# Kernel tuning notes

Hardware: AMD Instinct MI355X
Metric: run time of the kernel (lower is better)

The kernel has to match this reference:

```python
import jax, jax.numpy as jnp
import numpy as np

HIDDEN = 32  # hard-coded in the module


def _lstm_cell(x, h, c, W_ih, W_hh, b_ih, b_hh):
    # torch.nn.LSTMCell: gates in order i, f, g, o
    gates = x @ W_ih.T + b_ih + h @ W_hh.T + b_hh
    i, f, g, o = jnp.split(gates, 4, axis=-1)
    c_new = jax.nn.sigmoid(f) * c + jax.nn.sigmoid(i) * jnp.tanh(g)
    h_new = jax.nn.sigmoid(o) * jnp.tanh(c_new)
    return h_new, c_new


def setup_inputs() -> dict:
    key = jax.random.key(0)
    ks = jax.random.split(key, 11)
    B, T, d, len_out = 256, 1024, 8, 10
    s = 0.05
    return {
        "input": jax.random.normal(ks[0], (B, T, d), dtype=jnp.float32),
        "W_ih1": jax.random.normal(ks[1], (4 * HIDDEN, d), dtype=jnp.float32) * s,
        "W_hh1": jax.random.normal(ks[2], (4 * HIDDEN, HIDDEN), dtype=jnp.float32) * s,
        "b_ih1": jax.random.normal(ks[3], (4 * HIDDEN,), dtype=jnp.float32) * s,
        "b_hh1": jax.random.normal(ks[4], (4 * HIDDEN,), dtype=jnp.float32) * s,
        "W_ih2": jax.random.normal(ks[5], (4 * HIDDEN, HIDDEN), dtype=jnp.float32) * s,
        "W_hh2": jax.random.normal(ks[6], (4 * HIDDEN, HIDDEN), dtype=jnp.float32) * s,
        "b_ih2": jax.random.normal(ks[7], (4 * HIDDEN,), dtype=jnp.float32) * s,
        "b_hh2": jax.random.normal(ks[8], (4 * HIDDEN,), dtype=jnp.float32) * s,
        "W_lin": jax.random.normal(ks[9], (d * len_out, HIDDEN), dtype=jnp.float32) * s,
        "b_lin": jax.random.normal(ks[10], (d * len_out,), dtype=jnp.float32) * s,
    }


def reference(input, W_ih1, W_hh1, b_ih1, b_hh1, W_ih2, W_hh2, b_ih2, b_hh2, W_lin, b_lin):
    B, T, d = input.shape
    len_out = W_lin.shape[0] // d

    def step(carry, x_t):
        h1, c1, h2, c2 = carry
        h1, c1 = _lstm_cell(x_t, h1, c1, W_ih1, W_hh1, b_ih1, b_hh1)
        h2, c2 = _lstm_cell(h1, h2, c2, W_ih2, W_hh2, b_ih2, b_hh2)
        out = h2 @ W_lin.T + b_lin  # [B, d*len_out]
        return (h1, c1, h2, c2), out

    z = jnp.zeros((B, HIDDEN), dtype=input.dtype)
    init = (z, z, z, z)
    xs = jnp.swapaxes(input, 0, 1)  # [T, B, d]
    _, outs = jax.lax.scan(step, init, xs)  # [T, B, d*len_out]
    outs = jnp.swapaxes(outs, 0, 1)  # [B, T, d*len_out]
    return outs.reshape(B, T, d, len_out)
```

## Files before the change

kernel.cpp:

```cpp
#include <hip/hip_runtime.h>

#define TT  1024
#define DIN 8

__device__ __forceinline__ float fsig(float x) {
    float e = __builtin_amdgcn_exp2f(-1.4426950408889634f * x);
    return __builtin_amdgcn_rcpf(1.0f + e);
}
__device__ __forceinline__ float ftanh_(float x) {
    float e = __builtin_amdgcn_exp2f(-2.8853900817779268f * x);
    return 2.0f * __builtin_amdgcn_rcpf(1.0f + e) - 1.0f;
}
template<int CTRL>
__device__ __forceinline__ float dppf(float v) {
    return __uint_as_float((unsigned)__builtin_amdgcn_update_dpp(
        0, (int)__float_as_uint(v), CTRL, 0xF, 0xF, true));
}
__device__ __forceinline__ void bar_lgkm() {
    asm volatile("s_waitcnt lgkmcnt(0)\n\ts_barrier" ::: "memory");
}

__global__ void __launch_bounds__(512, 2)
lstm_pipe8(const float* __restrict__ x,
           const float* __restrict__ Wih1, const float* __restrict__ Whh1,
           const float* __restrict__ bih1, const float* __restrict__ bhh1,
           const float* __restrict__ Wih2, const float* __restrict__ Whh2,
           const float* __restrict__ bih2, const float* __restrict__ bhh2,
           const float* __restrict__ Wlin, const float* __restrict__ blin,
           float* __restrict__ out)
{
    const int tid  = threadIdx.x;
    const int wv   = tid >> 6;
    const int l    = tid & 63;
    const int part = l & 1;
    const int g    = (l >> 1) & 3;
    const int ul   = l >> 3;
    const int b    = blockIdx.x;
    const bool isL1 = (wv < 4);
    const int  wu   = isL1 ? wv : (wv - 4);
    const int  unit = wu*8 + ul;
    const int  R    = g*32 + unit;
    const bool isg  = (g == 2);

    __shared__ float hb1[2][32];
    __shared__ float hb2[2][32];
    if (tid < 64)       ((float*)hb1)[tid]      = 0.f;
    else if (tid < 128) ((float*)hb2)[tid - 64] = 0.f;

    float wg[20];
    float wg2[32];
    float wl[16];
    float bias = 0.f, obias = 0.f;
    int ocol = 0;

    if (isL1) {
        const float* wsrc = Whh1 + R*32 + part*16;
#pragma unroll
        for (int qq = 0; qq < 4; ++qq) {
            float4 v = reinterpret_cast<const float4*>(wsrc)[qq];
            wg[4*qq]=v.x; wg[4*qq+1]=v.y; wg[4*qq+2]=v.z; wg[4*qq+3]=v.w;
        }
        float4 xv = *reinterpret_cast<const float4*>(Wih1 + R*DIN + part*4);
        wg[16]=xv.x; wg[17]=xv.y; wg[18]=xv.z; wg[19]=xv.w;
        if (!part) bias = bih1[R] + bhh1[R];
        ocol = wu*20 + (l >> 1);
        const int oc = (l < 40) ? ocol : 79;
        const float* osrc = Wlin + oc*32 + part*16;
#pragma unroll
        for (int qq = 0; qq < 4; ++qq) {
            float4 v = reinterpret_cast<const float4*>(osrc)[qq];
            wl[4*qq]=v.x; wl[4*qq+1]=v.y; wl[4*qq+2]=v.z; wl[4*qq+3]=v.w;
        }
        if (!part) obias = blin[oc];
    } else {
        const float* wsrc = part ? (Wih2 + R*32) : (Whh2 + R*32);
#pragma unroll
        for (int qq = 0; qq < 8; ++qq) {
            float4 v = reinterpret_cast<const float4*>(wsrc)[qq];
            wg2[4*qq]=v.x; wg2[4*qq+1]=v.y; wg2[4*qq+2]=v.z; wg2[4*qq+3]=v.w;
        }
        if (!part) bias = bih2[R] + bhh2[R];
    }

    float c = 0.f;

    const float* __restrict__ xb = x   + (size_t)b * (TT*DIN);
    float* __restrict__ outb     = out + (size_t)b * (TT*80);

    float4 xcur;
    if (isL1) xcur = *reinterpret_cast<const float4*>(xb + part*4);

    bar_lgkm();

#pragma unroll 1
    for (int t = 0; t <= TT + 1; ++t) {
        const int pm1 = (t - 1) & 1;
        const int p0  = t & 1;

        if (isL1) {
            const float* hin = &hb1[pm1][part << 4];
            const float* hob = &hb2[p0][part << 4];
            float4 hg[4], ho[4];
#pragma unroll
            for (int qq = 0; qq < 4; ++qq) hg[qq] = reinterpret_cast<const float4*>(hin)[qq];
#pragma unroll
            for (int qq = 0; qq < 4; ++qq) ho[qq] = reinterpret_cast<const float4*>(hob)[qq];

            if (t < TT) {
                float a0 = bias, a1 = 0.f, a2 = 0.f, a3 = 0.f;
#pragma unroll
                for (int qq = 0; qq < 4; ++qq) {
                    a0 += wg[4*qq]  *hg[qq].x; a1 += wg[4*qq+1]*hg[qq].y;
                    a2 += wg[4*qq+2]*hg[qq].z; a3 += wg[4*qq+3]*hg[qq].w;
                }
                a0 += wg[16]*xcur.x; a1 += wg[17]*xcur.y;
                a2 += wg[18]*xcur.z; a3 += wg[19]*xcur.w;
                const int tn = (t + 1 < TT) ? (t + 1) : (TT - 1);
                xcur = *reinterpret_cast<const float4*>(xb + tn*DIN + part*4);

                float sum  = (a0 + a1) + (a2 + a3);
                float full = sum + dppf<0xB1>(sum);
                float u  = isg ? (full + full) : full;
                float S  = fsig(u);
                float av = isg ? (S + S - 1.0f) : S;
                float itg = dppf<0x114>(av) * av;
                float fv  = dppf<0x112>(av);
                c = fv * c + itg;
                float so  = dppf<0x102>(av);
                float hv  = so * ftanh_(c);
                if ((l & 7) == 4) hb1[p0][unit] = hv;
            }
            if (t >= 2) {
                float o0 = obias, o1 = 0.f, o2 = 0.f, o3 = 0.f;
#pragma unroll
                for (int qq = 0; qq < 4; ++qq) {
                    o0 += wl[4*qq]  *ho[qq].x; o1 += wl[4*qq+1]*ho[qq].y;
                    o2 += wl[4*qq+2]*ho[qq].z; o3 += wl[4*qq+3]*ho[qq].w;
                }
                float osum  = (o0 + o1) + (o2 + o3);
                float ofull = osum + dppf<0xB1>(osum);
                if (!part && l < 40)
                    outb[(size_t)(t - 2)*80 + ocol] = ofull;
            }
        } else {
            if (t >= 1 && t <= TT) {
                const float* hin = part ? &hb1[pm1][0] : &hb2[p0][0];
                float a0 = bias, a1 = 0.f, a2 = 0.f, a3 = 0.f;
#pragma unroll
                for (int qq = 0; qq < 8; ++qq) {
                    float4 v = reinterpret_cast<const float4*>(hin)[qq];
                    a0 += wg2[4*qq]  *v.x; a1 += wg2[4*qq+1]*v.y;
                    a2 += wg2[4*qq+2]*v.z; a3 += wg2[4*qq+3]*v.w;
                }
                float sum  = (a0 + a1) + (a2 + a3);
                float full = sum + dppf<0xB1>(sum);
                float u  = isg ? (full + full) : full;
                float S  = fsig(u);
                float av = isg ? (S + S - 1.0f) : S;
                float itg = dppf<0x114>(av) * av;
                float fv  = dppf<0x112>(av);
                c = fv * c + itg;
                float so  = dppf<0x102>(av);
                float hv  = so * ftanh_(c);
                if ((l & 7) == 4) hb2[pm1][unit] = hv;
            }
        }

        bar_lgkm();
    }
}

extern "C" void kernel_launch(void* const* d_in, const int* in_sizes, int n_in,
                              void* d_out, int out_size, void* d_ws, size_t ws_size,
                              hipStream_t stream) {
    const float* x    = (const float*)d_in[0];
    const float* Wih1 = (const float*)d_in[1];
    const float* Whh1 = (const float*)d_in[2];
    const float* bih1 = (const float*)d_in[3];
    const float* bhh1 = (const float*)d_in[4];
    const float* Wih2 = (const float*)d_in[5];
    const float* Whh2 = (const float*)d_in[6];
    const float* bih2 = (const float*)d_in[7];
    const float* bhh2 = (const float*)d_in[8];
    const float* Wlin = (const float*)d_in[9];
    const float* blin = (const float*)d_in[10];

    const int B = in_sizes[0] / (TT * DIN);

    hipLaunchKernelGGL(lstm_pipe8, dim3(B), dim3(512), 0, stream,
                       x, Wih1, Whh1, bih1, bhh1,
                       Wih2, Whh2, bih2, bhh2, Wlin, blin,
                       (float*)d_out);
}
```

Before: 464.8 us.

## Restructure LSTM kernel into per-wave roles handling two batch elements per block

Each 512-thread block now processes two batch elements, with four waves per element split into roles: a single wave for layer 1, two waves for layer 2, and one wave for the output projection. Layer 1 keeps its hidden state in registers and broadcasts it with readlane, so its recurrence no longer round-trips through LDS. The time loop is unrolled by two with ping-pong buffers. The aim is to shorten the per-step critical path and halve the grid, at the cost of more registers and more readlane work per step.

```diff
diff --git a/kernel.cpp b/kernel.cpp
--- a/kernel.cpp
+++ b/kernel.cpp
@@ -10,6 +10,9 @@
 __device__ __forceinline__ float ftanh_(float x) {
     float e = __builtin_amdgcn_exp2f(-2.8853900817779268f * x);
     return 2.0f * __builtin_amdgcn_rcpf(1.0f + e) - 1.0f;
+}
+__device__ __forceinline__ float bcastf(float v, int k) {
+    return __uint_as_float((unsigned)__builtin_amdgcn_readlane((int)__float_as_uint(v), k));
 }
 template<int CTRL>
 __device__ __forceinline__ float dppf(float v) {
@@ -19,9 +22,100 @@
 __device__ __forceinline__ void bar_lgkm() {
     asm volatile("s_waitcnt lgkmcnt(0)\n\ts_barrier" ::: "memory");
 }
+__device__ __forceinline__ void row32g(const float* __restrict__ p, float* r) {
+#pragma unroll
+    for (int qq = 0; qq < 8; ++qq) {
+        float4 v = reinterpret_cast<const float4*>(p)[qq];
+        r[4*qq]=v.x; r[4*qq+1]=v.y; r[4*qq+2]=v.z; r[4*qq+3]=v.w;
+    }
+}
+__device__ __forceinline__ void lds32(const float* p, float* r) {
+#pragma unroll
+    for (int qq = 0; qq < 8; ++qq) {
+        float4 v = reinterpret_cast<const float4*>(p)[qq];
+        r[4*qq]=v.x; r[4*qq+1]=v.y; r[4*qq+2]=v.z; r[4*qq+3]=v.w;
+    }
+}
+
+#define L1STEP(X0, X1, PAR)                                                   \
+    {                                                                         \
+        float p0a = bq0, p0b = 0.f, p1a = bq1, p1b = 0.f;                     \
+        _Pragma("unroll")                                                     \
+        for (int k = 0; k < 32; k += 2) {                                     \
+            p0a += wh0[k]*hs[k];   p0b += wh0[k+1]*hs[k+1];                   \
+            p1a += wh1[k]*hs[k];   p1b += wh1[k+1]*hs[k+1];                   \
+        }                                                                     \
+        p0a += wx0[0]*X0.x; p0b += wx0[1]*X0.y;                               \
+        p0a += wx0[2]*X0.z; p0b += wx0[3]*X0.w;                               \
+        p0a += wx0[4]*X1.x; p0b += wx0[5]*X1.y;                               \
+        p0a += wx0[6]*X1.z; p0b += wx0[7]*X1.w;                               \
+        p1a += wx1[0]*X0.x; p1b += wx1[1]*X0.y;                               \
+        p1a += wx1[2]*X0.z; p1b += wx1[3]*X0.w;                               \
+        p1a += wx1[4]*X1.x; p1b += wx1[5]*X1.y;                               \
+        p1a += wx1[6]*X1.z; p1b += wx1[7]*X1.w;                               \
+        float pp0 = p0a + p0b, pp1 = p1a + p1b;                               \
+        float A  = fsig(pp0);                                                 \
+        float uu = q ? pp1 : (pp1 + pp1);                                     \
+        float S  = fsig(uu);                                                  \
+        float Bv = q ? S : (S + S - 1.0f);                                    \
+        float An = dppf<0xB1>(A), Bn = dppf<0xB1>(Bv);                        \
+        float si = q ? An : A,  sf = q ? A  : An;                             \
+        float tg = q ? Bn : Bv, so = q ? Bv : Bn;                             \
+        c1 = sf * c1 + si * tg;                                               \
+        float h1v = so * ftanh_(c1);                                          \
+        if (!q) hb1[elem][PAR][j] = h1v;                                      \
+        _Pragma("unroll")                                                     \
+        for (int k = 0; k < 32; ++k) hs[k] = bcastf(h1v, 2*k);                \
+    }
+
+#define L2STEP(PT)                                                            \
+    {                                                                         \
+        float h1l = hb1[elem][PT][l & 31];                                    \
+        float h2r_[32];                                                       \
+        lds32(&hb2[elem][(PT)^1][0], h2r_);                                   \
+        float h1s_[32];                                                       \
+        _Pragma("unroll")                                                     \
+        for (int k = 0; k < 32; ++k) h1s_[k] = bcastf(h1l, k);                \
+        float a0 = bq, a1 = 0.f, a2 = 0.f, a3 = 0.f;                          \
+        _Pragma("unroll")                                                     \
+        for (int k = 0; k < 32; k += 4) {                                     \
+            a0 += w2[k]  *h1s_[k];   a1 += w2[k+1]*h1s_[k+1];                 \
+            a2 += w2[k+2]*h1s_[k+2]; a3 += w2[k+3]*h1s_[k+3];                 \
+        }                                                                     \
+        _Pragma("unroll")                                                     \
+        for (int k = 0; k < 32; k += 4) {                                     \
+            a0 += u2[k]  *h2r_[k];   a1 += u2[k+1]*h2r_[k+1];                 \
+            a2 += u2[k+2]*h2r_[k+2]; a3 += u2[k+3]*h2r_[k+3];                 \
+        }                                                                     \
+        float gg = (a0 + a1) + (a2 + a3);                                     \
+        float uu = isg ? (gg + gg) : gg;                                      \
+        float S  = fsig(uu);                                                  \
+        float av = isg ? (S + S - 1.0f) : S;                                  \
+        float siq = dppf<0x00>(av);                                           \
+        float sfq = dppf<0x55>(av);                                           \
+        float tgq = dppf<0xAA>(av);                                           \
+        float soq = dppf<0xFF>(av);                                           \
+        c2 = sfq * c2 + siq * tgq;                                            \
+        float h2v = soq * ftanh_(c2);                                         \
+        if (g == 0) hb2[elem][PT][u] = h2v;                                   \
+    }
+
+#define OUTSTEP(TAU, PT)                                                      \
+    {                                                                         \
+        float h2r_[32];                                                       \
+        lds32(&hb2[elem][PT][0], h2r_);                                       \
+        float o0 = bo0, o1 = 0.f, po0 = bo1, po1 = 0.f;                       \
+        _Pragma("unroll")                                                     \
+        for (int k = 0; k < 32; k += 2) {                                     \
+            o0  += wl0[k]*h2r_[k];  o1  += wl0[k+1]*h2r_[k+1];                \
+            po0 += wl1[k]*h2r_[k];  po1 += wl1[k+1]*h2r_[k+1];                \
+        }                                                                     \
+        outb[(size_t)(TAU)*80 + c0] = o0 + o1;                                \
+        if (l < 16) outb[(size_t)(TAU)*80 + 64 + l] = po0 + po1;              \
+    }
 
 __global__ void __launch_bounds__(512, 2)
-lstm_pipe8(const float* __restrict__ x,
+lstm_roles(const float* __restrict__ x,
            const float* __restrict__ Wih1, const float* __restrict__ Whh1,
            const float* __restrict__ bih1, const float* __restrict__ bhh1,
            const float* __restrict__ Wih2, const float* __restrict__ Whh2,
@@ -32,140 +126,103 @@
     const int tid  = threadIdx.x;
     const int wv   = tid >> 6;
     const int l    = tid & 63;
-    const int part = l & 1;
-    const int g    = (l >> 1) & 3;
-    const int ul   = l >> 3;
-    const int b    = blockIdx.x;
-    const bool isL1 = (wv < 4);
-    const int  wu   = isL1 ? wv : (wv - 4);
-    const int  unit = wu*8 + ul;
-    const int  R    = g*32 + unit;
-    const bool isg  = (g == 2);
-
-    __shared__ float hb1[2][32];
-    __shared__ float hb2[2][32];
-    if (tid < 64)       ((float*)hb1)[tid]      = 0.f;
-    else if (tid < 128) ((float*)hb2)[tid - 64] = 0.f;
-
-    float wg[20];
-    float wg2[32];
-    float wl[16];
-    float bias = 0.f, obias = 0.f;
-    int ocol = 0;
-
-    if (isL1) {
-        const float* wsrc = Whh1 + R*32 + part*16;
-#pragma unroll
-        for (int qq = 0; qq < 4; ++qq) {
-            float4 v = reinterpret_cast<const float4*>(wsrc)[qq];
-            wg[4*qq]=v.x; wg[4*qq+1]=v.y; wg[4*qq+2]=v.z; wg[4*qq+3]=v.w;
-        }
-        float4 xv = *reinterpret_cast<const float4*>(Wih1 + R*DIN + part*4);
-        wg[16]=xv.x; wg[17]=xv.y; wg[18]=xv.z; wg[19]=xv.w;
-        if (!part) bias = bih1[R] + bhh1[R];
-        ocol = wu*20 + (l >> 1);
-        const int oc = (l < 40) ? ocol : 79;
-        const float* osrc = Wlin + oc*32 + part*16;
-#pragma unroll
-        for (int qq = 0; qq < 4; ++qq) {
-            float4 v = reinterpret_cast<const float4*>(osrc)[qq];
-            wl[4*qq]=v.x; wl[4*qq+1]=v.y; wl[4*qq+2]=v.z; wl[4*qq+3]=v.w;
-        }
-        if (!part) obias = blin[oc];
-    } else {
-        const float* wsrc = part ? (Wih2 + R*32) : (Whh2 + R*32);
-#pragma unroll
-        for (int qq = 0; qq < 8; ++qq) {
-            float4 v = reinterpret_cast<const float4*>(wsrc)[qq];
-            wg2[4*qq]=v.x; wg2[4*qq+1]=v.y; wg2[4*qq+2]=v.z; wg2[4*qq+3]=v.w;
-        }
-        if (!part) bias = bih2[R] + bhh2[R];
-    }
-
-    float c = 0.f;
+    const int role = wv & 3;
+    const int elem = wv >> 2;
+    const int b    = blockIdx.x * 2 + elem;
+
+    __shared__ __align__(16) float hb1[2][2][32];
+    __shared__ __align__(16) float hb2[2][2][32];
+    if (tid < 128)      ((float*)hb1)[tid]       = 0.f;
+    else if (tid < 256) ((float*)hb2)[tid - 128] = 0.f;
 
     const float* __restrict__ xb = x   + (size_t)b * (TT*DIN);
     float* __restrict__ outb     = out + (size_t)b * (TT*80);
 
-    float4 xcur;
-    if (isL1) xcur = *reinterpret_cast<const float4*>(xb + part*4);
-
-    bar_lgkm();
+    if (role == 0) {
+        const int q = l & 1, j = l >> 1;
+        const int r0 = q ? (32 + j) : j;
+        const int r1 = q ? (96 + j) : (64 + j);
+        float wx0[8], wx1[8];
+#pragma unroll
+        for (int k = 0; k < 8; ++k) { wx0[k] = Wih1[r0*8+k]; wx1[k] = Wih1[r1*8+k]; }
+        float wh0[32], wh1[32];
+        row32g(Whh1 + r0*32, wh0); row32g(Whh1 + r1*32, wh1);
+        const float bq0 = bih1[r0] + bhh1[r0];
+        const float bq1 = bih1[r1] + bhh1[r1];
+        float hs[32];
+#pragma unroll
+        for (int k = 0; k < 32; ++k) hs[k] = 0.f;
+        float c1 = 0.f;
+        float4 xA0 = reinterpret_cast<const float4*>(xb)[0];
+        float4 xA1 = reinterpret_cast<const float4*>(xb)[1];
+        float4 xB0 = reinterpret_cast<const float4*>(xb)[2];
+        float4 xB1 = reinterpret_cast<const float4*>(xb)[3];
+
+        bar_lgkm();
 
 #pragma unroll 1
-    for (int t = 0; t <= TT + 1; ++t) {
-        const int pm1 = (t - 1) & 1;
-        const int p0  = t & 1;
-
-        if (isL1) {
-            const float* hin = &hb1[pm1][part << 4];
-            const float* hob = &hb2[p0][part << 4];
-            float4 hg[4], ho[4];
-#pragma unroll
-            for (int qq = 0; qq < 4; ++qq) hg[qq] = reinterpret_cast<const float4*>(hin)[qq];
-#pragma unroll
-            for (int qq = 0; qq < 4; ++qq) ho[qq] = reinterpret_cast<const float4*>(hob)[qq];
-
-            if (t < TT) {
-                float a0 = bias, a1 = 0.f, a2 = 0.f, a3 = 0.f;
-#pragma unroll
-                for (int qq = 0; qq < 4; ++qq) {
-                    a0 += wg[4*qq]  *hg[qq].x; a1 += wg[4*qq+1]*hg[qq].y;
-                    a2 += wg[4*qq+2]*hg[qq].z; a3 += wg[4*qq+3]*hg[qq].w;
-                }
-                a0 += wg[16]*xcur.x; a1 += wg[17]*xcur.y;
-                a2 += wg[18]*xcur.z; a3 += wg[19]*xcur.w;
-                const int tn = (t + 1 < TT) ? (t + 1) : (TT - 1);
-                xcur = *reinterpret_cast<const float4*>(xb + tn*DIN + part*4);
-
-                float sum  = (a0 + a1) + (a2 + a3);
-                float full = sum + dppf<0xB1>(sum);
-                float u  = isg ? (full + full) : full;
-                float S  = fsig(u);
-                float av = isg ? (S + S - 1.0f) : S;
-                float itg = dppf<0x114>(av) * av;
-                float fv  = dppf<0x112>(av);
-                c = fv * c + itg;
-                float so  = dppf<0x102>(av);
-                float hv  = so * ftanh_(c);
-                if ((l & 7) == 4) hb1[p0][unit] = hv;
+        for (int tp = 0; tp < TT/2; ++tp) {
+            const int te = 2*tp;
+            L1STEP(xA0, xA1, 0)
+            {
+                const int tn = (te + 2 <= TT - 1) ? (te + 2) : 0;
+                xA0 = reinterpret_cast<const float4*>(xb + tn*DIN)[0];
+                xA1 = reinterpret_cast<const float4*>(xb + tn*DIN)[1];
             }
-            if (t >= 2) {
-                float o0 = obias, o1 = 0.f, o2 = 0.f, o3 = 0.f;
-#pragma unroll
-                for (int qq = 0; qq < 4; ++qq) {
-                    o0 += wl[4*qq]  *ho[qq].x; o1 += wl[4*qq+1]*ho[qq].y;
-                    o2 += wl[4*qq+2]*ho[qq].z; o3 += wl[4*qq+3]*ho[qq].w;
-                }
-                float osum  = (o0 + o1) + (o2 + o3);
-                float ofull = osum + dppf<0xB1>(osum);
-                if (!part && l < 40)
-                    outb[(size_t)(t - 2)*80 + ocol] = ofull;
+            bar_lgkm();
+            L1STEP(xB0, xB1, 1)
+            {
+                const int tn = (te + 3 <= TT - 1) ? (te + 3) : 0;
+                xB0 = reinterpret_cast<const float4*>(xb + tn*DIN)[0];
+                xB1 = reinterpret_cast<const float4*>(xb + tn*DIN)[1];
             }
-        } else {
-            if (t >= 1 && t <= TT) {
-                const float* hin = part ? &hb1[pm1][0] : &hb2[p0][0];
-                float a0 = bias, a1 = 0.f, a2 = 0.f, a3 = 0.f;
-#pragma unroll
-                for (int qq = 0; qq < 8; ++qq) {
-                    float4 v = reinterpret_cast<const float4*>(hin)[qq];
-                    a0 += wg2[4*qq]  *v.x; a1 += wg2[4*qq+1]*v.y;
-                    a2 += wg2[4*qq+2]*v.z; a3 += wg2[4*qq+3]*v.w;
-                }
-                float sum  = (a0 + a1) + (a2 + a3);
-                float full = sum + dppf<0xB1>(sum);
-                float u  = isg ? (full + full) : full;
-                float S  = fsig(u);
-                float av = isg ? (S + S - 1.0f) : S;
-                float itg = dppf<0x114>(av) * av;
-                float fv  = dppf<0x112>(av);
-                c = fv * c + itg;
-                float so  = dppf<0x102>(av);
-                float hv  = so * ftanh_(c);
-                if ((l & 7) == 4) hb2[pm1][unit] = hv;
-            }
+            bar_lgkm();
         }
-
+        bar_lgkm();
+        bar_lgkm();
+    } else if (role <= 2) {
+        const int g  = l & 3;
+        const int u  = (role - 1)*16 + (l >> 2);
+        const int R  = g*32 + u;
+        const bool isg = (g == 2);
+        float w2[32], u2[32];
+        row32g(Wih2 + R*32, w2); row32g(Whh2 + R*32, u2);
+        const float bq = bih2[R] + bhh2[R];
+        float c2 = 0.f;
+
+        bar_lgkm();
+
+#pragma unroll 1
+        for (int tp = 0; tp < TT/2; ++tp) {
+            if (tp > 0) L2STEP(1)
+            bar_lgkm();
+            L2STEP(0)
+            bar_lgkm();
+        }
+        L2STEP(1)
+        bar_lgkm();
+        bar_lgkm();
+    } else {
+        const int c0  = l;
+        const int c1c = (l < 16) ? (64 + l) : 79;
+        float wl0[32], wl1[32];
+        row32g(Wlin + c0*32,  wl0);
+        row32g(Wlin + c1c*32, wl1);
+        const float bo0 = blin[c0], bo1 = blin[c1c];
+
+        bar_lgkm();
+
+#pragma unroll 1
+        for (int tp = 0; tp < TT/2; ++tp) {
+            const int te = 2*tp;
+            if (tp >= 1) OUTSTEP(te - 2, 0)
+            bar_lgkm();
+            if (tp >= 1) OUTSTEP(te - 1, 1)
+            bar_lgkm();
+        }
+        OUTSTEP(TT - 2, 0)
+        bar_lgkm();
+        OUTSTEP(TT - 1, 1)
         bar_lgkm();
     }
 }
@@ -186,8 +243,9 @@
     const float* blin = (const float*)d_in[10];
 
     const int B = in_sizes[0] / (TT * DIN);
-
-    hipLaunchKernelGGL(lstm_pipe8, dim3(B), dim3(512), 0, stream,
+    const int G = B / 2;
+
+    hipLaunchKernelGGL(lstm_roles, dim3(G), dim3(512), 0, stream,
                        x, Wih1, Whh1, bih1, bhh1,
                        Wih2, Whh2, bih2, bhh2, Wlin, blin,
                        (float*)d_out);
```

Result: slower. 769.6 us (+65.6%).
